# Kernel optimization log

Hardware: AMD Instinct MI355X
Metric: run time of the kernel (lower is better)

The kernel has to match this reference:

```python
import jax, jax.numpy as jnp
import numpy as np

B, T, C, H = 8, 1024, 1024, 16
D = C // H  # head dim = 64

def setup_inputs() -> dict:
    key = jax.random.key(0)
    k1, k2, k3 = jax.random.split(key, 3)
    x = jax.random.normal(k1, (B, T, C), dtype=jnp.float32)
    W_attn = jax.random.normal(k2, (C, 3 * C), dtype=jnp.float32) * (1.0 / np.sqrt(C))
    W_proj = jax.random.normal(k3, (C, C), dtype=jnp.float32) * (1.0 / np.sqrt(C))
    # Llama RoPE frequencies: base^(-2i/D)
    omega = (10000.0 ** (-jnp.arange(0, D, 2, dtype=jnp.float32) / D))  # [D/2]
    return {"x": x, "W_attn": W_attn, "W_proj": W_proj, "omega": omega}

def _apply_rope(x, omega):
    # x: [B, T, H, D]; omega: [D/2]
    t = x.shape[1]
    ang = jnp.arange(t, dtype=x.dtype)[:, None] * omega[None, :]  # [T, D/2]
    cos = jnp.cos(ang)[None, :, None, :]  # [1, T, 1, D/2]
    sin = jnp.sin(ang)[None, :, None, :]
    d2 = x.shape[-1] // 2
    x1, x2 = x[..., :d2], x[..., d2:]
    return jnp.concatenate([x1 * cos - x2 * sin, x2 * cos + x1 * sin], axis=-1)

def reference(x, W_attn, W_proj, omega):
    b, t, c = x.shape
    qkv = jnp.einsum('btc,cd->btd', x, W_attn)  # fused QKV projection
    q, k, v = jnp.split(qkv, 3, axis=-1)
    q = q.reshape(b, t, H, D)
    k = k.reshape(b, t, H, D)
    v = v.reshape(b, t, H, D)
    q = _apply_rope(q, omega)
    k = _apply_rope(k, omega)
    # non-causal SDPA
    scale = 1.0 / jnp.sqrt(jnp.asarray(D, dtype=x.dtype))
    scores = jnp.einsum('bqhd,bkhd->bhqk', q, k) * scale
    probs = jax.nn.softmax(scores, axis=-1)
    y = jnp.einsum('bhqk,bkhd->bqhd', probs, v).reshape(b, t, c)
    return jnp.einsum('btc,cd->btd', y, W_proj)
```

## Files before the change

kernel.cpp:

```cpp
#include <hip/hip_runtime.h>
#include <hip/hip_bf16.h>
#include <stdint.h>


typedef __attribute__((ext_vector_type(8))) short short8;
typedef __attribute__((ext_vector_type(4))) float floatx4;
typedef __attribute__((ext_vector_type(2))) unsigned int uint2v;

#define DEV static __device__ __forceinline__

#if __has_builtin(__builtin_amdgcn_exp2f)
#define EXP2(x) __builtin_amdgcn_exp2f(x)
#else
#define EXP2(x) exp2f(x)
#endif

DEV uint16_t f2bf(float f) {
  union { float f; uint32_t i; } v; v.f = f;
  uint32_t u = v.i;
  return (uint16_t)((u + 0x7fffu + ((u >> 16) & 1u)) >> 16);
}

DEV uint32_t pkbf(float a, float b) {
  __hip_bfloat162 h = __float22bfloat162_rn(make_float2(a, b));
  union { __hip_bfloat162 h; uint32_t u; } v; v.h = h;
  return v.u;
}

DEV void async_load16(const uint16_t* g, uint16_t* l) {
  __builtin_amdgcn_global_load_lds(
      (const __attribute__((address_space(1))) void*)g,
      (__attribute__((address_space(3))) void*)l, 16, 0, 0);
}

__global__ __launch_bounds__(256) void prep(
    const float* __restrict__ x, const float* __restrict__ W_attn,
    const float* __restrict__ W_proj, const float* __restrict__ omega,
    uint16_t* __restrict__ xb, uint16_t* __restrict__ Wt_attn,
    uint16_t* __restrict__ Wt_proj, float2* __restrict__ tab) {
  __shared__ uint16_t tile[64][65];
  const int blk = blockIdx.x, tid = threadIdx.x;
  if (blk < 4096) {
    const size_t base = ((size_t)blk * 256 + tid) * 8;
    floatx4 a = *(const floatx4*)(x + base);
    floatx4 b = *(const floatx4*)(x + base + 4);
    short8 s;
    s[0] = (short)f2bf(a[0]); s[1] = (short)f2bf(a[1]);
    s[2] = (short)f2bf(a[2]); s[3] = (short)f2bf(a[3]);
    s[4] = (short)f2bf(b[0]); s[5] = (short)f2bf(b[1]);
    s[6] = (short)f2bf(b[2]); s[7] = (short)f2bf(b[3]);
    *(short8*)(xb + base) = s;
  } else if (blk < 5120) {
    const float* in;
    uint16_t* out;
    int R = 1024, Ccols, bx, by;
    if (blk < 4864) {
      const int idx = blk - 4096;
      in = W_attn; out = Wt_attn; Ccols = 3072;
      bx = idx % 48; by = idx / 48;
    } else {
      const int idx = blk - 4864;
      in = W_proj; out = Wt_proj; Ccols = 1024;
      bx = idx % 16; by = idx / 16;
    }
    const int tx = tid & 63, ty = tid >> 6;
    const int c0 = bx * 64, r0 = by * 64;
    #pragma unroll
    for (int i = 0; i < 64; i += 4)
      tile[ty + i][tx] = f2bf(in[(size_t)(r0 + ty + i) * Ccols + c0 + tx]);
    __syncthreads();
    #pragma unroll
    for (int i = 0; i < 64; i += 4)
      out[(size_t)(c0 + ty + i) * R + r0 + tx] = tile[tx][ty + i];
  } else {
    const int idx = (blk - 5120) * 256 + tid;
    const int t = idx >> 5, d = idx & 31;
    float s, c;
    sincosf((float)t * omega[d], &s, &c);
    tab[idx] = make_float2(c, s);
  }
}

__global__ __launch_bounds__(256) void gemm_qkv(
    const uint16_t* __restrict__ A, const uint16_t* __restrict__ Bt,
    const float2* __restrict__ tab,
    uint16_t* __restrict__ Qr, uint16_t* __restrict__ Kr, uint16_t* __restrict__ Vt) {
  __shared__ uint16_t As[128 * 64];
  __shared__ uint16_t Bs[128 * 64];
  const int tid = threadIdx.x;
  const int wave = tid >> 6, lane = tid & 63;
  const int l15 = lane & 15, quad = lane >> 4;
  const int row0 = blockIdx.y * 128, col0 = blockIdx.x * 128;
  const int wr = (wave >> 1) * 64, wc = (wave & 1) * 64;
  const int K = 1024;
  const int sw = l15 & 7;

  floatx4 acc[4][4];
  const floatx4 z4 = {0.f, 0.f, 0.f, 0.f};
  #pragma unroll
  for (int mi = 0; mi < 4; mi++)
    #pragma unroll
    for (int ni = 0; ni < 4; ni++) acc[mi][ni] = z4;

  for (int k0 = 0; k0 < K; k0 += 64) {
    __syncthreads();
    #pragma unroll
    for (int i = 0; i < 4; i++) {
      const int e = i * 256 + tid;
      const int r = e >> 3;
      const int j = (e & 7) ^ (r & 7);
      async_load16(A + (size_t)(row0 + r) * K + k0 + j * 8, As + e * 8);
      async_load16(Bt + (size_t)(col0 + r) * K + k0 + j * 8, Bs + e * 8);
    }
    __syncthreads();
    #pragma unroll
    for (int ks = 0; ks < 2; ks++) {
      short8 af[4], bfr[4];
      #pragma unroll
      for (int mi = 0; mi < 4; mi++)
        af[mi] = *(const short8*)(&As[(wr + mi * 16 + l15) * 64 +
                                      (((ks * 4 + quad) ^ sw) * 8)]);
      #pragma unroll
      for (int ni = 0; ni < 4; ni++)
        bfr[ni] = *(const short8*)(&Bs[(wc + ni * 16 + l15) * 64 +
                                       (((ks * 4 + quad) ^ sw) * 8)]);
      #pragma unroll
      for (int mi = 0; mi < 4; mi++)
        #pragma unroll
        for (int ni = 0; ni < 4; ni++)
          acc[mi][ni] = __builtin_amdgcn_mfma_f32_16x16x32_bf16(
              af[mi], bfr[ni], acc[mi][ni], 0, 0, 0);
    }
  }

  const int cblk = col0 + wc;
  const int region = cblk >> 10;
  const int h = (cblk & 1023) >> 6;
  const int b = row0 >> 10;
  const int tbase = (row0 & 1023) + wr;
  const size_t bh = (size_t)b * 16 + h;

  if (region < 2) {
    uint16_t* dst = (region == 0) ? Qr : Kr;
    const float scl = (region == 0) ? 0.125f * 1.44269504088896f : 1.0f;
    #pragma unroll
    for (int mi = 0; mi < 4; mi++)
      #pragma unroll
      for (int r = 0; r < 4; r++) {
        const int t = tbase + mi * 16 + quad * 4 + r;
        const size_t base = (bh * 1024 + t) * 64;
        const float2 cs0 = tab[t * 32 + l15];
        const float2 cs1 = tab[t * 32 + l15 + 16];
        {
          float x1 = acc[mi][0][r], x2 = acc[mi][2][r];
          dst[base + l15]      = f2bf((x1 * cs0.x - x2 * cs0.y) * scl);
          dst[base + l15 + 32] = f2bf((x2 * cs0.x + x1 * cs0.y) * scl);
        }
        {
          float x1 = acc[mi][1][r], x2 = acc[mi][3][r];
          dst[base + 16 + l15]      = f2bf((x1 * cs1.x - x2 * cs1.y) * scl);
          dst[base + 16 + l15 + 32] = f2bf((x2 * cs1.x + x1 * cs1.y) * scl);
        }
      }
  } else {
    #pragma unroll
    for (int mi = 0; mi < 4; mi++)
      #pragma unroll
      for (int ni = 0; ni < 4; ni++) {
        const int d = ni * 16 + l15;
        #pragma unroll
        for (int r = 0; r < 4; r++) {
          const int t = tbase + mi * 16 + quad * 4 + r;
          Vt[bh * 65536 + (size_t)d * 1024 + t] = f2bf(acc[mi][ni][r]);
        }
      }
  }
}

__global__ __launch_bounds__(256) void gemm_out(
    const uint16_t* __restrict__ A, const uint16_t* __restrict__ Bt,
    float* __restrict__ Cmat, int M, int N, int K) {
  __shared__ uint16_t As[128 * 64];
  __shared__ uint16_t Bs[128 * 64];
  const int tid = threadIdx.x;
  const int wave = tid >> 6, lane = tid & 63;
  const int l15 = lane & 15, quad = lane >> 4;
  const int row0 = blockIdx.y * 128, col0 = blockIdx.x * 128;
  const int wr = (wave >> 1) * 64, wc = (wave & 1) * 64;
  const int sw = l15 & 7;

  floatx4 acc[4][4];
  const floatx4 z4 = {0.f, 0.f, 0.f, 0.f};
  #pragma unroll
  for (int mi = 0; mi < 4; mi++)
    #pragma unroll
    for (int ni = 0; ni < 4; ni++) acc[mi][ni] = z4;

  for (int k0 = 0; k0 < K; k0 += 64) {
    __syncthreads();
    #pragma unroll
    for (int i = 0; i < 4; i++) {
      const int e = i * 256 + tid;
      const int r = e >> 3;
      const int j = (e & 7) ^ (r & 7);
      async_load16(A + (size_t)(row0 + r) * K + k0 + j * 8, As + e * 8);
      async_load16(Bt + (size_t)(col0 + r) * K + k0 + j * 8, Bs + e * 8);
    }
    __syncthreads();
    #pragma unroll
    for (int ks = 0; ks < 2; ks++) {
      short8 af[4], bfr[4];
      #pragma unroll
      for (int mi = 0; mi < 4; mi++)
        af[mi] = *(const short8*)(&As[(wr + mi * 16 + l15) * 64 +
                                      (((ks * 4 + quad) ^ sw) * 8)]);
      #pragma unroll
      for (int ni = 0; ni < 4; ni++)
        bfr[ni] = *(const short8*)(&Bs[(wc + ni * 16 + l15) * 64 +
                                       (((ks * 4 + quad) ^ sw) * 8)]);
      #pragma unroll
      for (int mi = 0; mi < 4; mi++)
        #pragma unroll
        for (int ni = 0; ni < 4; ni++)
          acc[mi][ni] = __builtin_amdgcn_mfma_f32_16x16x32_bf16(
              af[mi], bfr[ni], acc[mi][ni], 0, 0, 0);
    }
  }
  #pragma unroll
  for (int mi = 0; mi < 4; mi++)
    #pragma unroll
    for (int ni = 0; ni < 4; ni++) {
      const int col = col0 + wc + ni * 16 + l15;
      #pragma unroll
      for (int r = 0; r < 4; r++) {
        const int row = row0 + wr + mi * 16 + quad * 4 + r;
        Cmat[(size_t)row * N + col] = acc[mi][ni][r];
      }
    }
}

#define FLD 72

__global__ __launch_bounds__(256) void flash_attn(
    const uint16_t* __restrict__ Qr, const uint16_t* __restrict__ Kr,
    const uint16_t* __restrict__ Vt, uint16_t* __restrict__ Y) {
  __shared__ uint16_t Ks[64 * 64];
  __shared__ uint16_t Vs[64 * 64];
  __shared__ uint16_t Ps[128 * FLD];
  const int tid = threadIdx.x;
  const int wv = tid >> 6, lane = tid & 63;
  const int l15 = lane & 15, quad = lane >> 4;
  const int sw = l15 & 7;
  const int bh = blockIdx.x & 127, qt = blockIdx.x >> 7;
  const int b = bh >> 4, h = bh & 15;
  const int q0 = qt * 128;
  const uint16_t* Qbh = Qr + (size_t)bh * 1024 * 64;
  const uint16_t* Kbh = Kr + (size_t)bh * 1024 * 64;
  const uint16_t* Vbh = Vt + (size_t)bh * 64 * 1024;

  short8 bq[2][2];
  #pragma unroll
  for (int g = 0; g < 2; g++)
    #pragma unroll
    for (int ks = 0; ks < 2; ks++)
      bq[g][ks] = *(const short8*)(Qbh +
          (size_t)(q0 + wv * 32 + g * 16 + l15) * 64 + ks * 32 + quad * 8);

  float psum[2] = {0.f, 0.f};
  const floatx4 z4 = {0.f, 0.f, 0.f, 0.f};
  floatx4 oacc[2][4];
  #pragma unroll
  for (int g = 0; g < 2; g++)
    #pragma unroll
    for (int mi = 0; mi < 4; mi++) oacc[g][mi] = z4;

  for (int kt = 0; kt < 16; kt++) {
    __syncthreads();
    #pragma unroll
    for (int i = 0; i < 2; i++) {
      const int e = i * 256 + tid;
      const int r = e >> 3;
      const int j = (e & 7) ^ (r & 7);
      async_load16(Kbh + (size_t)(kt * 64 + r) * 64 + j * 8, Ks + e * 8);
      async_load16(Vbh + (size_t)r * 1024 + kt * 64 + j * 8, Vs + e * 8);
    }
    __syncthreads();

    #pragma unroll
    for (int g = 0; g < 2; g++) {
      const int qrow = wv * 32 + g * 16 + l15;
      floatx4 sacc[4];
      #pragma unroll
      for (int ni = 0; ni < 4; ni++) {
        sacc[ni] = z4;
        #pragma unroll
        for (int ks = 0; ks < 2; ks++) {
          short8 ak = *(const short8*)(&Ks[(ni * 16 + l15) * 64 +
                                           (((ks * 4 + quad) ^ sw) * 8)]);
          sacc[ni] = __builtin_amdgcn_mfma_f32_16x16x32_bf16(ak, bq[g][ks], sacc[ni], 0, 0, 0);
        }
      }
      #pragma unroll
      for (int ni = 0; ni < 4; ni++) {
        float p0 = EXP2(sacc[ni][0]), p1 = EXP2(sacc[ni][1]);
        float p2 = EXP2(sacc[ni][2]), p3 = EXP2(sacc[ni][3]);
        psum[g] += (p0 + p1) + (p2 + p3);
        uint2v pk; pk[0] = pkbf(p0, p1); pk[1] = pkbf(p2, p3);
        *(uint2v*)(&Ps[qrow * FLD + ni * 16 + quad * 4]) = pk;
      }
      short8 bp[2];
      #pragma unroll
      for (int ks = 0; ks < 2; ks++)
        bp[ks] = *(const short8*)(&Ps[qrow * FLD + ks * 32 + quad * 8]);
      #pragma unroll
      for (int mi = 0; mi < 4; mi++) {
        #pragma unroll
        for (int ks = 0; ks < 2; ks++) {
          short8 av = *(const short8*)(&Vs[(mi * 16 + l15) * 64 +
                                           (((ks * 4 + quad) ^ sw) * 8)]);
          oacc[g][mi] = __builtin_amdgcn_mfma_f32_16x16x32_bf16(av, bp[ks], oacc[g][mi], 0, 0, 0);
        }
      }
    }
  }

  #pragma unroll
  for (int g = 0; g < 2; g++) {
    float l_tot = psum[g];
    l_tot += __shfl_xor(l_tot, 16, 64);
    l_tot += __shfl_xor(l_tot, 32, 64);
    const float linv = 1.0f / l_tot;
    const int t = q0 + wv * 32 + g * 16 + l15;
    #pragma unroll
    for (int mi = 0; mi < 4; mi++) {
      uint2v yk;
      yk[0] = pkbf(oacc[g][mi][0] * linv, oacc[g][mi][1] * linv);
      yk[1] = pkbf(oacc[g][mi][2] * linv, oacc[g][mi][3] * linv);
      *(uint2v*)(Y + (size_t)(b * 1024 + t) * 1024 + h * 64 + mi * 16 + quad * 4) = yk;
    }
  }
}

extern "C" void kernel_launch(void* const* d_in, const int* in_sizes, int n_in,
                              void* d_out, int out_size, void* d_ws, size_t ws_size,
                              hipStream_t stream) {
  const float* x      = (const float*)d_in[0];
  const float* W_attn = (const float*)d_in[1];
  const float* W_proj = (const float*)d_in[2];
  const float* omega  = (const float*)d_in[3];
  float* out = (float*)d_out;

  uint16_t* wsp     = (uint16_t*)d_ws;
  uint16_t* xb      = wsp;
  uint16_t* Wt_attn = xb + (size_t)8192 * 1024;
  uint16_t* Wt_proj = Wt_attn + (size_t)3072 * 1024;
  uint16_t* Qr      = Wt_proj + (size_t)1024 * 1024;
  uint16_t* Kr      = Qr + (size_t)128 * 1024 * 64;
  uint16_t* Vt      = Kr + (size_t)128 * 1024 * 64;
  float2*   ropet   = (float2*)(Vt + (size_t)128 * 1024 * 64);
  uint16_t* Y       = xb;

  prep<<<5248, 256, 0, stream>>>(x, W_attn, W_proj, omega, xb, Wt_attn, Wt_proj, ropet);
  gemm_qkv<<<dim3(24, 64), 256, 0, stream>>>(xb, Wt_attn, ropet, Qr, Kr, Vt);
  flash_attn<<<1024, 256, 0, stream>>>(Qr, Kr, Vt, Y);
  gemm_out<<<dim3(8, 64), 256, 0, stream>>>(Y, Wt_proj, out, 8192, 1024, 1024);
}
```

Before: 248.3 us.

## Pipeline both GEMMs with triple-buffered async loads and 256x128 tiles

Replaces the two synchronous single-buffer GEMM main loops with a shared core that uses 512-thread blocks, 256x128 output tiles and a three-stage LDS ring. Async global-to-LDS loads for tile k+2 are issued while MFMAs run on tile k, with explicit vmcnt waits, barriers and setprio around the MFMA bursts. The goal is to hide global-load latency and cut barrier stalls. In exchange LDS use is much larger (about 144KB per block), and the hand-counted waits are fragile.

```diff
diff --git a/kernel.cpp b/kernel.cpp
--- a/kernel.cpp
+++ b/kernel.cpp
@@ -81,63 +81,137 @@
   }
 }
 
-__global__ __launch_bounds__(256) void gemm_qkv(
+DEV void gemm_core8(const uint16_t* __restrict__ Ag,
+                    const uint16_t* __restrict__ Bg,
+                    int row0, int col0,
+                    uint16_t* As, uint16_t* Bs, floatx4 (&acc)[4][4]) {
+  const int tid = threadIdx.x;
+  const int wave = tid >> 6, lane = tid & 63;
+  const int l15 = lane & 15, quad = lane >> 4;
+  const int wrow = wave >> 1, wcol = wave & 1;
+  const int sw = l15 & 7;
+  const int K = 1024;
+
+  size_t aoff[4], boff[2];
+  #pragma unroll
+  for (int i = 0; i < 4; i++) {
+    const int e = i * 512 + tid;
+    const int r = e >> 3, c = e & 7, j = c ^ (r & 7);
+    aoff[i] = (size_t)(row0 + r) * K + j * 8;
+  }
+  #pragma unroll
+  for (int i = 0; i < 2; i++) {
+    const int e = i * 512 + tid;
+    const int r = e >> 3, c = e & 7, j = c ^ (r & 7);
+    boff[i] = (size_t)(col0 + r) * K + j * 8;
+  }
+
+  #pragma unroll
+  for (int t = 0; t < 2; t++) {
+    #pragma unroll
+    for (int i = 0; i < 2; i++)
+      async_load16(Bg + boff[i] + (size_t)t * 64, Bs + t * 8192 + (i * 512 + tid) * 8);
+    #pragma unroll
+    for (int i = 0; i < 4; i++)
+      async_load16(Ag + aoff[i] + (size_t)t * 64, As + t * 16384 + (i * 512 + tid) * 8);
+  }
+
+  const floatx4 z4 = {0.f, 0.f, 0.f, 0.f};
+  #pragma unroll
+  for (int mi = 0; mi < 4; mi++)
+    #pragma unroll
+    for (int ni = 0; ni < 4; ni++) acc[mi][ni] = z4;
+
+  asm volatile("s_waitcnt vmcnt(6)" ::: "memory");
+  __builtin_amdgcn_s_barrier();
+
+  int qa = 0, q2 = 2;
+  const int arow = wrow * 64 + l15;
+  const int brow = wcol * 64 + l15;
+  for (int kt = 0; kt < 16; ++kt) {
+    const uint16_t* Aq = As + qa * 16384;
+    const uint16_t* Bq = Bs + qa * 8192;
+    uint16_t* As2 = As + q2 * 16384;
+    uint16_t* Bs2 = Bs + q2 * 8192;
+    const size_t k2 = (size_t)(kt + 2) * 64;
+
+    short8 af[4], bfr[4];
+    #pragma unroll
+    for (int mi = 0; mi < 4; mi++)
+      af[mi] = *(const short8*)(Aq + (arow + mi * 16) * 64 + ((quad ^ sw) * 8));
+    #pragma unroll
+    for (int ni = 0; ni < 4; ni++)
+      bfr[ni] = *(const short8*)(Bq + (brow + ni * 16) * 64 + ((quad ^ sw) * 8));
+    if (kt < 14) {
+      #pragma unroll
+      for (int i = 0; i < 2; i++)
+        async_load16(Bg + boff[i] + k2, Bs2 + (i * 512 + tid) * 8);
+      #pragma unroll
+      for (int i = 0; i < 2; i++)
+        async_load16(Ag + aoff[i] + k2, As2 + (i * 512 + tid) * 8);
+    }
+    __builtin_amdgcn_s_barrier();
+    asm volatile("s_waitcnt lgkmcnt(0)" ::: "memory");
+    __builtin_amdgcn_s_setprio(1);
+    #pragma unroll
+    for (int mi = 0; mi < 4; mi++)
+      #pragma unroll
+      for (int ni = 0; ni < 4; ni++)
+        acc[mi][ni] = __builtin_amdgcn_mfma_f32_16x16x32_bf16(
+            af[mi], bfr[ni], acc[mi][ni], 0, 0, 0);
+    __builtin_amdgcn_s_setprio(0);
+    __builtin_amdgcn_s_barrier();
+
+    #pragma unroll
+    for (int mi = 0; mi < 4; mi++)
+      af[mi] = *(const short8*)(Aq + (arow + mi * 16) * 64 + (((4 + quad) ^ sw) * 8));
+    #pragma unroll
+    for (int ni = 0; ni < 4; ni++)
+      bfr[ni] = *(const short8*)(Bq + (brow + ni * 16) * 64 + (((4 + quad) ^ sw) * 8));
+    if (kt < 14) {
+      #pragma unroll
+      for (int i = 2; i < 4; i++)
+        async_load16(Ag + aoff[i] + k2, As2 + (i * 512 + tid) * 8);
+      asm volatile("s_waitcnt vmcnt(6)" ::: "memory");
+    } else if (kt == 14) {
+      asm volatile("s_waitcnt vmcnt(0)" ::: "memory");
+    }
+    __builtin_amdgcn_s_barrier();
+    asm volatile("s_waitcnt lgkmcnt(0)" ::: "memory");
+    __builtin_amdgcn_s_setprio(1);
+    #pragma unroll
+    for (int mi = 0; mi < 4; mi++)
+      #pragma unroll
+      for (int ni = 0; ni < 4; ni++)
+        acc[mi][ni] = __builtin_amdgcn_mfma_f32_16x16x32_bf16(
+            af[mi], bfr[ni], acc[mi][ni], 0, 0, 0);
+    __builtin_amdgcn_s_setprio(0);
+    __builtin_amdgcn_s_barrier();
+
+    qa = (qa == 2) ? 0 : qa + 1;
+    q2 = (q2 == 2) ? 0 : q2 + 1;
+  }
+}
+
+__global__ __launch_bounds__(512) void gemm_qkv(
     const uint16_t* __restrict__ A, const uint16_t* __restrict__ Bt,
     const float2* __restrict__ tab,
     uint16_t* __restrict__ Qr, uint16_t* __restrict__ Kr, uint16_t* __restrict__ Vt) {
-  __shared__ uint16_t As[128 * 64];
-  __shared__ uint16_t Bs[128 * 64];
+  __shared__ __align__(16) uint16_t As[3 * 256 * 64];
+  __shared__ __align__(16) uint16_t Bs[3 * 128 * 64];
+  const int row0 = blockIdx.y * 256, col0 = blockIdx.x * 128;
+  floatx4 acc[4][4];
+  gemm_core8(A, Bt, row0, col0, As, Bs, acc);
+
   const int tid = threadIdx.x;
   const int wave = tid >> 6, lane = tid & 63;
   const int l15 = lane & 15, quad = lane >> 4;
-  const int row0 = blockIdx.y * 128, col0 = blockIdx.x * 128;
-  const int wr = (wave >> 1) * 64, wc = (wave & 1) * 64;
-  const int K = 1024;
-  const int sw = l15 & 7;
-
-  floatx4 acc[4][4];
-  const floatx4 z4 = {0.f, 0.f, 0.f, 0.f};
-  #pragma unroll
-  for (int mi = 0; mi < 4; mi++)
-    #pragma unroll
-    for (int ni = 0; ni < 4; ni++) acc[mi][ni] = z4;
-
-  for (int k0 = 0; k0 < K; k0 += 64) {
-    __syncthreads();
-    #pragma unroll
-    for (int i = 0; i < 4; i++) {
-      const int e = i * 256 + tid;
-      const int r = e >> 3;
-      const int j = (e & 7) ^ (r & 7);
-      async_load16(A + (size_t)(row0 + r) * K + k0 + j * 8, As + e * 8);
-      async_load16(Bt + (size_t)(col0 + r) * K + k0 + j * 8, Bs + e * 8);
-    }
-    __syncthreads();
-    #pragma unroll
-    for (int ks = 0; ks < 2; ks++) {
-      short8 af[4], bfr[4];
-      #pragma unroll
-      for (int mi = 0; mi < 4; mi++)
-        af[mi] = *(const short8*)(&As[(wr + mi * 16 + l15) * 64 +
-                                      (((ks * 4 + quad) ^ sw) * 8)]);
-      #pragma unroll
-      for (int ni = 0; ni < 4; ni++)
-        bfr[ni] = *(const short8*)(&Bs[(wc + ni * 16 + l15) * 64 +
-                                       (((ks * 4 + quad) ^ sw) * 8)]);
-      #pragma unroll
-      for (int mi = 0; mi < 4; mi++)
-        #pragma unroll
-        for (int ni = 0; ni < 4; ni++)
-          acc[mi][ni] = __builtin_amdgcn_mfma_f32_16x16x32_bf16(
-              af[mi], bfr[ni], acc[mi][ni], 0, 0, 0);
-    }
-  }
-
-  const int cblk = col0 + wc;
+  const int cblk = col0 + (wave & 1) * 64;
   const int region = cblk >> 10;
   const int h = (cblk & 1023) >> 6;
-  const int b = row0 >> 10;
-  const int tbase = (row0 & 1023) + wr;
+  const int rr = row0 + (wave >> 1) * 64;
+  const int b = rr >> 10;
+  const int tbase = rr & 1023;
   const size_t bh = (size_t)b * 16 + h;
 
   if (region < 2) {
@@ -177,63 +251,26 @@
   }
 }
 
-__global__ __launch_bounds__(256) void gemm_out(
+__global__ __launch_bounds__(512) void gemm_out(
     const uint16_t* __restrict__ A, const uint16_t* __restrict__ Bt,
     float* __restrict__ Cmat, int M, int N, int K) {
-  __shared__ uint16_t As[128 * 64];
-  __shared__ uint16_t Bs[128 * 64];
+  __shared__ __align__(16) uint16_t As[3 * 256 * 64];
+  __shared__ __align__(16) uint16_t Bs[3 * 128 * 64];
+  const int row0 = blockIdx.y * 256, col0 = blockIdx.x * 128;
+  floatx4 acc[4][4];
+  gemm_core8(A, Bt, row0, col0, As, Bs, acc);
+
   const int tid = threadIdx.x;
   const int wave = tid >> 6, lane = tid & 63;
   const int l15 = lane & 15, quad = lane >> 4;
-  const int row0 = blockIdx.y * 128, col0 = blockIdx.x * 128;
-  const int wr = (wave >> 1) * 64, wc = (wave & 1) * 64;
-  const int sw = l15 & 7;
-
-  floatx4 acc[4][4];
-  const floatx4 z4 = {0.f, 0.f, 0.f, 0.f};
   #pragma unroll
   for (int mi = 0; mi < 4; mi++)
     #pragma unroll
-    for (int ni = 0; ni < 4; ni++) acc[mi][ni] = z4;
-
-  for (int k0 = 0; k0 < K; k0 += 64) {
-    __syncthreads();
-    #pragma unroll
-    for (int i = 0; i < 4; i++) {
-      const int e = i * 256 + tid;
-      const int r = e >> 3;
-      const int j = (e & 7) ^ (r & 7);
-      async_load16(A + (size_t)(row0 + r) * K + k0 + j * 8, As + e * 8);
-      async_load16(Bt + (size_t)(col0 + r) * K + k0 + j * 8, Bs + e * 8);
-    }
-    __syncthreads();
-    #pragma unroll
-    for (int ks = 0; ks < 2; ks++) {
-      short8 af[4], bfr[4];
-      #pragma unroll
-      for (int mi = 0; mi < 4; mi++)
-        af[mi] = *(const short8*)(&As[(wr + mi * 16 + l15) * 64 +
-                                      (((ks * 4 + quad) ^ sw) * 8)]);
-      #pragma unroll
-      for (int ni = 0; ni < 4; ni++)
-        bfr[ni] = *(const short8*)(&Bs[(wc + ni * 16 + l15) * 64 +
-                                       (((ks * 4 + quad) ^ sw) * 8)]);
-      #pragma unroll
-      for (int mi = 0; mi < 4; mi++)
-        #pragma unroll
-        for (int ni = 0; ni < 4; ni++)
-          acc[mi][ni] = __builtin_amdgcn_mfma_f32_16x16x32_bf16(
-              af[mi], bfr[ni], acc[mi][ni], 0, 0, 0);
-    }
-  }
-  #pragma unroll
-  for (int mi = 0; mi < 4; mi++)
-    #pragma unroll
     for (int ni = 0; ni < 4; ni++) {
-      const int col = col0 + wc + ni * 16 + l15;
+      const int col = col0 + (wave & 1) * 64 + ni * 16 + l15;
       #pragma unroll
       for (int r = 0; r < 4; r++) {
-        const int row = row0 + wr + mi * 16 + quad * 4 + r;
+        const int row = row0 + (wave >> 1) * 64 + mi * 16 + quad * 4 + r;
         Cmat[(size_t)row * N + col] = acc[mi][ni][r];
       }
     }
@@ -361,7 +398,7 @@
   uint16_t* Y       = xb;
 
   prep<<<5248, 256, 0, stream>>>(x, W_attn, W_proj, omega, xb, Wt_attn, Wt_proj, ropet);
-  gemm_qkv<<<dim3(24, 64), 256, 0, stream>>>(xb, Wt_attn, ropet, Qr, Kr, Vt);
+  gemm_qkv<<<dim3(24, 32), 512, 0, stream>>>(xb, Wt_attn, ropet, Qr, Kr, Vt);
   flash_attn<<<1024, 256, 0, stream>>>(Qr, Kr, Vt, Y);
-  gemm_out<<<dim3(8, 64), 256, 0, stream>>>(Y, Wt_proj, out, 8192, 1024, 1024);
-}
+  gemm_out<<<dim3(8, 32), 512, 0, stream>>>(Y, Wt_proj, out, 8192, 1024, 1024);
+}
```

After: 243.7 us. About the same (-1.8%).
